# Kernel optimization log

Hardware: AMD Instinct MI355X
Metric: run time of the kernel (lower is better)

The kernel has to match this reference:

```python
import jax, jax.numpy as jnp
import numpy as np

ASSIGN_TEMP = 0.1
BATCH_SIZE = 16
NUM_PROTOTYPES = 1024
EMBD_DIM = 512


def setup_inputs() -> dict:
    key = jax.random.key(0)
    k1, k2 = jax.random.split(key)
    feature_maps = jax.random.normal(k1, (BATCH_SIZE, EMBD_DIM, 64, 64), dtype=jnp.float32)
    prototypes = jax.random.normal(k2, (1, NUM_PROTOTYPES, EMBD_DIM), dtype=jnp.float32)
    return {"feature_maps": feature_maps, "prototypes": prototypes}


def reference(feature_maps, prototypes):
    # assign_nearest_clusters
    bs, c, h, w = feature_maps.shape
    K = prototypes.shape[1]
    # [N, c] pixel embeddings (channels-last flatten, as movedim(1,3).reshape)
    x = feature_maps.transpose(0, 2, 3, 1).reshape(-1, c)
    p = prototypes[0]  # [K, c]
    d2 = (jnp.sum(x * x, axis=1, keepdims=True)
          + jnp.sum(p * p, axis=1)[None, :]
          - 2.0 * (x @ p.T))
    dist = jnp.sqrt(jnp.maximum(d2, 0.0))  # [N, K]
    sims = jax.nn.softmax(-dist / ASSIGN_TEMP, axis=1)  # [N, K]
    sims = sims.reshape(bs, h, w, K).transpose(0, 3, 1, 2)  # [bs, K, h, w]
    nearest = jnp.argmax(sims, axis=1)  # [bs, h, w]
    onehot = jax.nn.one_hot(nearest, K, dtype=jnp.int32)  # [bs, h, w, K]
    counts = onehot.sum(axis=(1, 2))  # [bs, K] pixels per prototype
    mask = (counts > 3).sum()
    return sims, mask.astype(jnp.float32) / BATCH_SIZE
```

## Files before the change

### kernel.cpp

```cpp
#include <hip/hip_runtime.h>
#include <hip/hip_bf16.h>
#include <stdint.h>

typedef _Float16 f16x8 __attribute__((ext_vector_type(8)));
typedef _Float16 f16x2 __attribute__((ext_vector_type(2)));
typedef float    f32x4 __attribute__((ext_vector_type(4)));

#define NPROTO 1024
#define EMB    512
#define NB     16
#define HW     4096
#define NPIX   (NB * HW)
#define INV_TEMP 10.0f
#define TPX    64
#define NTHR   1024

__global__ void prep_protos(const float* __restrict__ proto,
                            _Float16* __restrict__ Ph,
                            float* __restrict__ pnorm) {
    int k = blockIdx.x;
    int t = threadIdx.x;
    const float* src = proto + (size_t)k * EMB + t * 8;
    float4 v0 = ((const float4*)src)[0];
    float4 v1 = ((const float4*)src)[1];
    float sq = v0.x*v0.x + v0.y*v0.y + v0.z*v0.z + v0.w*v0.w
             + v1.x*v1.x + v1.y*v1.y + v1.z*v1.z + v1.w*v1.w;
    f16x8 h;
    h[0] = (_Float16)v0.x; h[1] = (_Float16)v0.y; h[2] = (_Float16)v0.z; h[3] = (_Float16)v0.w;
    h[4] = (_Float16)v1.x; h[5] = (_Float16)v1.y; h[6] = (_Float16)v1.z; h[7] = (_Float16)v1.w;
    *(f16x8*)(Ph + (size_t)k * EMB + t * 8) = h;
#pragma unroll
    for (int m = 1; m < 64; m <<= 1) sq += __shfl_xor(sq, m);
    if (t == 0) pnorm[k] = sq;
}

__global__ void zero_counts(int* __restrict__ counts) {
    int i = blockIdx.x * blockDim.x + threadIdx.x;
    if (i < NB * NPROTO) counts[i] = 0;
}

__global__ __launch_bounds__(NTHR)
void assign_main(const float* __restrict__ fm, const _Float16* __restrict__ Ph,
                 const float* __restrict__ pnorm, int* __restrict__ counts,
                 float* __restrict__ out) {
    __shared__ __align__(16) unsigned char smem[143360];
    unsigned char* Abuf = smem;
    unsigned char* Bbuf = smem + 131072;
    float* pn           = (float*)(smem + 139264);
    float* redmax = (float*)(smem);
    float* redsum = (float*)(smem + 4096);
    float* argv_  = (float*)(smem + 8192);
    int*   argk_  = (int*)  (smem + 12288);
    float* xnsum  = (float*)(smem + 16384);
    float* xn     = (float*)(smem + 20480);

    const int t    = threadIdx.x;
    const int lane = t & 63, wid = t >> 6;
    const int lrow = lane >> 4;
    const int lcol = lane & 15;

    const int n0  = blockIdx.x * TPX;
    const int b   = n0 >> 12;
    const int hw0 = n0 & 4095;

    pn[t] = pnorm[t];

    f32x4 acc[4][4];
#pragma unroll
    for (int i = 0; i < 4; ++i)
#pragma unroll
        for (int j = 0; j < 4; ++j)
#pragma unroll
            for (int e = 0; e < 4; ++e) acc[i][j][e] = 0.0f;

    const int bpx = t & 63;
    const int bc  = (t >> 6) << 1;
    const float* fmB = fm + (size_t)b * EMB * HW + hw0 + bpx;
    float sq = 0.0f;
    float bv0, bv1;

    auto stageA = [&](int cur, int ks) {
        const int c0 = ks * 32;
#pragma unroll
        for (int p = 0; p < 4; ++p) {
            int k  = p * 256 + wid * 16 + (lane >> 2);
            int cg = (lane & 3) ^ (k & 3);
            const _Float16* src = Ph + (size_t)k * EMB + c0 + cg * 8;
            __builtin_amdgcn_global_load_lds(
                (const __attribute__((address_space(1))) void*)src,
                (__attribute__((address_space(3))) void*)(Abuf + cur * 65536 + p * 16384 + wid * 1024),
                16, 0, 0);
        }
    };
    auto loadB = [&](int ks) {
        const float* p0 = fmB + (size_t)(ks * 32 + bc) * HW;
        bv0 = p0[0];
        bv1 = p0[HW];
    };
    auto writeB = [&](int cur) {
        sq += bv0 * bv0 + bv1 * bv1;
        f16x2 h; h[0] = (_Float16)bv0; h[1] = (_Float16)bv1;
        int slot = (bc >> 3) ^ (bpx & 3);
        *(f16x2*)(Bbuf + cur * 4096 + bpx * 64 + (slot << 4) + (bc & 7) * 2) = h;
    };

    stageA(0, 0);
    loadB(0);
    writeB(0);
    __syncthreads();

    int cur = 0;
    for (int ks = 0; ks < 16; ++ks) {
        if (ks < 15) {
            stageA(cur ^ 1, ks + 1);
            loadB(ks + 1);
        }
        f16x8 bf[4];
#pragma unroll
        for (int nf = 0; nf < 4; ++nf) {
            int px   = nf * 16 + lcol;
            int slot = lrow ^ (px & 3);
            bf[nf] = *(const f16x8*)(Bbuf + cur * 4096 + px * 64 + (slot << 4));
        }
#pragma unroll
        for (int mf = 0; mf < 4; ++mf) {
            int r    = wid * 64 + mf * 16 + lcol;
            int slot = lrow ^ (r & 3);
            f16x8 af = *(const f16x8*)(Abuf + cur * 65536 + r * 64 + (slot << 4));
#pragma unroll
            for (int nf = 0; nf < 4; ++nf)
                acc[mf][nf] = __builtin_amdgcn_mfma_f32_16x16x32_f16(af, bf[nf], acc[mf][nf], 0, 0, 0);
        }
        if (ks < 15) writeB(cur ^ 1);
        __syncthreads();
        cur ^= 1;
    }

    xnsum[(t >> 6) * 64 + bpx] = sq;
    __syncthreads();
    if (t < 64) {
        float s = 0.0f;
#pragma unroll
        for (int g = 0; g < 16; ++g) s += xnsum[g * 64 + t];
        xn[t] = s;
    }
    __syncthreads();

    float xnv[4];
#pragma unroll
    for (int nf = 0; nf < 4; ++nf) xnv[nf] = xn[nf * 16 + lcol];

    float lmax[4] = {-1e30f, -1e30f, -1e30f, -1e30f};
    float lav[4]  = {-1e30f, -1e30f, -1e30f, -1e30f};
    int   lak[4]  = {0, 0, 0, 0};
#pragma unroll
    for (int mf = 0; mf < 4; ++mf) {
#pragma unroll
        for (int nf = 0; nf < 4; ++nf) {
#pragma unroll
            for (int j = 0; j < 4; ++j) {
                int kidx = wid * 64 + mf * 16 + lrow * 4 + j;
                float d2 = xnv[nf] + pn[kidx] - 2.0f * acc[mf][nf][j];
                float lg = -INV_TEMP * sqrtf(fmaxf(d2, 0.0f));
                acc[mf][nf][j] = lg;
                if (lg > lav[nf]) { lav[nf] = lg; lak[nf] = kidx; }
                lmax[nf] = fmaxf(lmax[nf], lg);
            }
        }
    }
#pragma unroll
    for (int nf = 0; nf < 4; ++nf) {
#pragma unroll
        for (int m = 16; m <= 32; m <<= 1) {
            float ov = __shfl_xor(lav[nf], m);
            int   ok = __shfl_xor(lak[nf], m);
            if (ov > lav[nf] || (ov == lav[nf] && ok < lak[nf])) { lav[nf] = ov; lak[nf] = ok; }
            lmax[nf] = fmaxf(lmax[nf], __shfl_xor(lmax[nf], m));
        }
    }
    if (lane < 16) {
#pragma unroll
        for (int nf = 0; nf < 4; ++nf) {
            int idx = wid * 64 + nf * 16 + lane;
            redmax[idx] = lmax[nf];
            argv_[idx]  = lav[nf];
            argk_[idx]  = lak[nf];
        }
    }
    __syncthreads();

    float gmax[4];
#pragma unroll
    for (int nf = 0; nf < 4; ++nf) {
        int px = nf * 16 + lcol;
        float gm = -1e30f, gav = -1e30f;
        int gak = 0;
#pragma unroll
        for (int w = 0; w < 16; ++w) {
            gm = fmaxf(gm, redmax[w * 64 + px]);
            float av = argv_[w * 64 + px];
            int   ak = argk_[w * 64 + px];
            if (av > gav || (av == gav && ak < gak)) { gav = av; gak = ak; }
        }
        gmax[nf] = gm;
        if (wid == 0 && lane < 16) atomicAdd(&counts[b * NPROTO + gak], 1);

        float s = 0.0f;
#pragma unroll
        for (int mf = 0; mf < 4; ++mf)
#pragma unroll
            for (int j = 0; j < 4; ++j) {
                float e = __expf(acc[mf][nf][j] - gm);
                acc[mf][nf][j] = e;
                s += e;
            }
        s += __shfl_xor(s, 16);
        s += __shfl_xor(s, 32);
        if (lane < 16) redsum[wid * 64 + nf * 16 + lane] = s;
    }
    __syncthreads();

    const size_t obase = (size_t)b * NPROTO * HW + hw0;
#pragma unroll
    for (int nf = 0; nf < 4; ++nf) {
        int px = nf * 16 + lcol;
        float s = 0.0f;
#pragma unroll
        for (int w = 0; w < 16; ++w) s += redsum[w * 64 + px];
        float inv = 1.0f / s;
#pragma unroll
        for (int mf = 0; mf < 4; ++mf)
#pragma unroll
            for (int j = 0; j < 4; ++j) {
                int kidx = wid * 64 + mf * 16 + lrow * 4 + j;
                out[obase + (size_t)kidx * HW + px] = acc[mf][nf][j] * inv;
            }
    }
}

__global__ void finalize(const int* __restrict__ counts, float* __restrict__ out) {
    int t = threadIdx.x;
    int local = 0;
    for (int i = t; i < NB * NPROTO; i += 256) local += (counts[i] > 3) ? 1 : 0;
#pragma unroll
    for (int m = 1; m < 64; m <<= 1) local += __shfl_xor(local, m);
    __shared__ int wsum[4];
    if ((t & 63) == 0) wsum[t >> 6] = local;
    __syncthreads();
    if (t == 0) out[(size_t)NPIX * NPROTO] = (float)(wsum[0] + wsum[1] + wsum[2] + wsum[3]) / 16.0f;
}

extern "C" void kernel_launch(void* const* d_in, const int* in_sizes, int n_in,
                              void* d_out, int out_size, void* d_ws, size_t ws_size,
                              hipStream_t stream) {
    const float* fm    = (const float*)d_in[0];
    const float* proto = (const float*)d_in[1];
    float* out = (float*)d_out;

    char* ws = (char*)d_ws;
    _Float16* Ph     = (_Float16*)ws;
    float*    pnorm  = (float*)(ws + (size_t)NPROTO * EMB * 2);
    int*      counts = (int*)(ws + (size_t)NPROTO * EMB * 2 + 4096);

    prep_protos<<<NPROTO, 64, 0, stream>>>(proto, Ph, pnorm);
    zero_counts<<<(NB * NPROTO + 255) / 256, 256, 0, stream>>>(counts);
    assign_main<<<NPIX / TPX, NTHR, 0, stream>>>(fm, Ph, pnorm, counts, out);
    finalize<<<1, 256, 0, stream>>>(counts, out);
}
```

Measured before the change: 299.5 us.

## Split assignment into transpose, stats, and recompute-emit passes with coalesced output

Adds a pre-pass that transposes feature maps into a channels-last fp16 buffer along with pixel norms. A stats kernel then runs the GEMM to get the per-pixel max, inverse softmax sum and argmax counts, and an emit kernel recomputes the GEMM in 256x256 tiles, staging results through LDS so the output writes are coalesced float4 stores. The aim is to remove the poorly coalesced strided output stores and the scalar fp32 B loads of the fused kernel. The cost is a second full GEMM and a 64MB intermediate buffer. The new path runs only when the workspace is large enough, and the old fused kernel is kept as a fallback.

```diff
diff --git a/kernel.cpp b/kernel.cpp
--- a/kernel.cpp
+++ b/kernel.cpp
@@ -12,8 +12,6 @@
 #define HW     4096
 #define NPIX   (NB * HW)
 #define INV_TEMP 10.0f
-#define TPX    64
-#define NTHR   1024
 
 __global__ void prep_protos(const float* __restrict__ proto,
                             _Float16* __restrict__ Ph,
@@ -39,10 +37,314 @@
     if (i < NB * NPROTO) counts[i] = 0;
 }
 
-__global__ __launch_bounds__(NTHR)
-void assign_main(const float* __restrict__ fm, const _Float16* __restrict__ Ph,
-                 const float* __restrict__ pnorm, int* __restrict__ counts,
-                 float* __restrict__ out) {
+__global__ __launch_bounds__(1024)
+void p0_transpose(const float* __restrict__ fm, _Float16* __restrict__ Xh,
+                  float* __restrict__ xn) {
+    __shared__ __align__(16) unsigned char tile[128 * 1024];
+    __shared__ float xnpart[32 * 128];
+
+    const int t   = threadIdx.x;
+    const int b   = blockIdx.x >> 5;
+    const int px0 = (blockIdx.x & 31) * 128;
+
+    float sq0 = 0.f, sq1 = 0.f, sq2 = 0.f, sq3 = 0.f;
+    const int p4 = t & 31;
+#pragma unroll
+    for (int j = 0; j < 16; ++j) {
+        int f4 = j * 1024 + t;
+        int c  = f4 >> 5;
+        float4 v = *(const float4*)(fm + ((size_t)b * EMB + c) * HW + px0 + p4 * 4);
+        sq0 += v.x * v.x; sq1 += v.y * v.y; sq2 += v.z * v.z; sq3 += v.w * v.w;
+#pragma unroll
+        for (int i = 0; i < 4; ++i) {
+            int p = p4 * 4 + i;
+            float val = (i == 0) ? v.x : (i == 1) ? v.y : (i == 2) ? v.z : v.w;
+            int slot = (c >> 3) ^ ((p >> 2) & 63);
+            *(_Float16*)(tile + p * 1024 + slot * 16 + (c & 7) * 2) = (_Float16)val;
+        }
+    }
+    xnpart[(t >> 5) * 128 + p4 * 4 + 0] = sq0;
+    xnpart[(t >> 5) * 128 + p4 * 4 + 1] = sq1;
+    xnpart[(t >> 5) * 128 + p4 * 4 + 2] = sq2;
+    xnpart[(t >> 5) * 128 + p4 * 4 + 3] = sq3;
+    __syncthreads();
+
+    if (t < 128) {
+        float s = 0.f;
+#pragma unroll
+        for (int g = 0; g < 32; ++g) s += xnpart[g * 128 + t];
+        xn[b * HW + px0 + t] = s;
+    }
+    const int wid = t >> 6, lane = t & 63;
+#pragma unroll
+    for (int rr = 0; rr < 8; ++rr) {
+        int p = wid * 8 + rr;
+        int phys = lane ^ ((p >> 2) & 63);
+        f16x8 v = *(const f16x8*)(tile + p * 1024 + phys * 16);
+        *(f16x8*)(Xh + ((size_t)b * HW + px0 + p) * EMB + lane * 8) = v;
+    }
+}
+
+__global__ __launch_bounds__(1024, 4)
+void p1_stats(const _Float16* __restrict__ Xh, const _Float16* __restrict__ Ph,
+              const float* __restrict__ pnorm, const float* __restrict__ xn,
+              int* __restrict__ counts, float* __restrict__ m_g, float* __restrict__ rs_g) {
+    __shared__ __align__(16) unsigned char smem[143360];
+    unsigned char* Abuf = smem;
+    unsigned char* Bbuf = smem + 131072;
+    float* pn           = (float*)(smem + 139264);
+    float* redmax = (float*)(smem);
+    float* redsum = (float*)(smem + 4096);
+    float* argv_  = (float*)(smem + 8192);
+    int*   argk_  = (int*)  (smem + 12288);
+
+    const int t    = threadIdx.x;
+    const int lane = t & 63, wid = t >> 6;
+    const int lrow = lane >> 4, lcol = lane & 15;
+    const int n0   = blockIdx.x * 64;
+    const int b    = n0 >> 12;
+
+    pn[t] = pnorm[t];
+
+    f32x4 acc[4][4];
+#pragma unroll
+    for (int i = 0; i < 4; ++i)
+#pragma unroll
+        for (int j = 0; j < 4; ++j)
+#pragma unroll
+            for (int e = 0; e < 4; ++e) acc[i][j][e] = 0.0f;
+
+    auto stageA = [&](int cur, int ks) {
+        const int c0 = ks * 32;
+#pragma unroll
+        for (int p = 0; p < 4; ++p) {
+            int k  = p * 256 + wid * 16 + (lane >> 2);
+            int cg = (lane & 3) ^ (k & 3);
+            __builtin_amdgcn_global_load_lds(
+                (const __attribute__((address_space(1))) void*)(Ph + (size_t)k * EMB + c0 + cg * 8),
+                (__attribute__((address_space(3))) void*)(Abuf + cur * 65536 + p * 16384 + wid * 1024),
+                16, 0, 0);
+        }
+    };
+    auto stageB = [&](int cur, int ks) {
+        if (wid < 4) {
+            const int c0 = ks * 32;
+            int row = wid * 16 + (lane >> 2);
+            int cg  = (lane & 3) ^ (row & 3);
+            __builtin_amdgcn_global_load_lds(
+                (const __attribute__((address_space(1))) void*)(Xh + (size_t)(n0 + row) * EMB + c0 + cg * 8),
+                (__attribute__((address_space(3))) void*)(Bbuf + cur * 4096 + wid * 1024),
+                16, 0, 0);
+        }
+    };
+
+    stageA(0, 0); stageB(0, 0);
+    __syncthreads();
+
+    int cur = 0;
+    for (int ks = 0; ks < 16; ++ks) {
+        if (ks < 15) { stageA(cur ^ 1, ks + 1); stageB(cur ^ 1, ks + 1); }
+        f16x8 bf[4];
+#pragma unroll
+        for (int nf = 0; nf < 4; ++nf) {
+            int p = nf * 16 + lcol;
+            bf[nf] = *(const f16x8*)(Bbuf + cur * 4096 + p * 64 + ((lrow ^ (p & 3)) << 4));
+        }
+#pragma unroll
+        for (int mf = 0; mf < 4; ++mf) {
+            int r = wid * 64 + mf * 16 + lcol;
+            f16x8 af = *(const f16x8*)(Abuf + cur * 65536 + r * 64 + ((lrow ^ (r & 3)) << 4));
+#pragma unroll
+            for (int nf = 0; nf < 4; ++nf)
+                acc[mf][nf] = __builtin_amdgcn_mfma_f32_16x16x32_f16(af, bf[nf], acc[mf][nf], 0, 0, 0);
+        }
+        __syncthreads();
+        cur ^= 1;
+    }
+
+    float xnv[4];
+#pragma unroll
+    for (int nf = 0; nf < 4; ++nf) xnv[nf] = xn[n0 + nf * 16 + lcol];
+
+    float lmax[4] = {-1e30f, -1e30f, -1e30f, -1e30f};
+    float lav[4]  = {-1e30f, -1e30f, -1e30f, -1e30f};
+    int   lak[4]  = {0, 0, 0, 0};
+#pragma unroll
+    for (int mf = 0; mf < 4; ++mf)
+#pragma unroll
+        for (int nf = 0; nf < 4; ++nf)
+#pragma unroll
+            for (int j = 0; j < 4; ++j) {
+                int kidx = wid * 64 + mf * 16 + lrow * 4 + j;
+                float d2 = xnv[nf] + pn[kidx] - 2.0f * acc[mf][nf][j];
+                float lg = -INV_TEMP * sqrtf(fmaxf(d2, 0.0f));
+                acc[mf][nf][j] = lg;
+                if (lg > lav[nf]) { lav[nf] = lg; lak[nf] = kidx; }
+                lmax[nf] = fmaxf(lmax[nf], lg);
+            }
+#pragma unroll
+    for (int nf = 0; nf < 4; ++nf)
+#pragma unroll
+        for (int m = 16; m <= 32; m <<= 1) {
+            float ov = __shfl_xor(lav[nf], m);
+            int   ok = __shfl_xor(lak[nf], m);
+            if (ov > lav[nf] || (ov == lav[nf] && ok < lak[nf])) { lav[nf] = ov; lak[nf] = ok; }
+            lmax[nf] = fmaxf(lmax[nf], __shfl_xor(lmax[nf], m));
+        }
+    if (lane < 16)
+#pragma unroll
+        for (int nf = 0; nf < 4; ++nf) {
+            int idx = wid * 64 + nf * 16 + lane;
+            redmax[idx] = lmax[nf]; argv_[idx] = lav[nf]; argk_[idx] = lak[nf];
+        }
+    __syncthreads();
+
+#pragma unroll
+    for (int nf = 0; nf < 4; ++nf) {
+        int px = nf * 16 + lcol;
+        float gm = -1e30f, gav = -1e30f;
+        int gak = 0;
+#pragma unroll
+        for (int w = 0; w < 16; ++w) {
+            gm = fmaxf(gm, redmax[w * 64 + px]);
+            float av = argv_[w * 64 + px];
+            int   ak = argk_[w * 64 + px];
+            if (av > gav || (av == gav && ak < gak)) { gav = av; gak = ak; }
+        }
+        if (wid == 0 && lane < 16) atomicAdd(&counts[b * NPROTO + gak], 1);
+        float s = 0.0f;
+#pragma unroll
+        for (int mf = 0; mf < 4; ++mf)
+#pragma unroll
+            for (int j = 0; j < 4; ++j) s += __expf(acc[mf][nf][j] - gm);
+        s += __shfl_xor(s, 16);
+        s += __shfl_xor(s, 32);
+        if (lane < 16) redsum[wid * 64 + nf * 16 + lane] = s;
+    }
+    __syncthreads();
+
+    if (t < 64) {
+        float gm = -1e30f, s = 0.0f;
+#pragma unroll
+        for (int w = 0; w < 16; ++w) { gm = fmaxf(gm, redmax[w * 64 + t]); s += redsum[w * 64 + t]; }
+        m_g[n0 + t]  = gm;
+        rs_g[n0 + t] = 1.0f / s;
+    }
+}
+
+__global__ __launch_bounds__(1024, 4)
+void p2_emit(const _Float16* __restrict__ Xh, const _Float16* __restrict__ Ph,
+             const float* __restrict__ pnorm, const float* __restrict__ xn,
+             const float* __restrict__ m_g, const float* __restrict__ rs_g,
+             float* __restrict__ out) {
+    __shared__ __align__(16) unsigned char smem[139264];
+    unsigned char* Abuf = smem;
+    unsigned char* Bbuf = smem + 32768;
+    float* EP  = (float*)(smem + 65536);
+    float* pnl = (float*)(smem + 131072);
+    float* xnl = (float*)(smem + 135168);
+    float* ml  = (float*)(smem + 136192);
+    float* rsl = (float*)(smem + 137216);
+
+    const int t    = threadIdx.x;
+    const int lane = t & 63, wid = t >> 6;
+    const int kw = wid >> 2, pw = wid & 3;
+    const int lrow = lane >> 4, lcol = lane & 15;
+
+    const int b   = blockIdx.x >> 4;
+    const int pxc = (blockIdx.x & 15) * 256;
+    const int n0  = b * HW + pxc;
+
+    pnl[t] = pnorm[t];
+    if (t < 256) { xnl[t] = xn[n0 + t]; ml[t] = m_g[n0 + t]; rsl[t] = rs_g[n0 + t]; }
+
+    auto stage = [&](int cur, int kq, int cs) {
+        const int c0 = cs * 32;
+        int rl   = wid * 16 + (lane >> 2);
+        int slot = lane & 3;
+        int cgA  = slot ^ (rl & 3);
+        __builtin_amdgcn_global_load_lds(
+            (const __attribute__((address_space(1))) void*)(Ph + (size_t)(kq * 256 + rl) * EMB + c0 + cgA * 8),
+            (__attribute__((address_space(3))) void*)(Abuf + cur * 16384 + wid * 1024), 16, 0, 0);
+        __builtin_amdgcn_global_load_lds(
+            (const __attribute__((address_space(1))) void*)(Xh + (size_t)(n0 + rl) * EMB + c0 + cgA * 8),
+            (__attribute__((address_space(3))) void*)(Bbuf + cur * 16384 + wid * 1024), 16, 0, 0);
+    };
+
+    for (int kq = 0; kq < 4; ++kq) {
+        f32x4 acc[4][4];
+#pragma unroll
+        for (int i = 0; i < 4; ++i)
+#pragma unroll
+            for (int j = 0; j < 4; ++j)
+#pragma unroll
+                for (int e = 0; e < 4; ++e) acc[i][j][e] = 0.0f;
+
+        stage(0, kq, 0);
+        __syncthreads();
+        int cur = 0;
+        for (int cs = 0; cs < 16; ++cs) {
+            if (cs < 15) stage(cur ^ 1, kq, cs + 1);
+            f16x8 bf[4];
+#pragma unroll
+            for (int nf = 0; nf < 4; ++nf) {
+                int p = pw * 64 + nf * 16 + lcol;
+                bf[nf] = *(const f16x8*)(Bbuf + cur * 16384 + p * 64 + ((lrow ^ (p & 3)) << 4));
+            }
+#pragma unroll
+            for (int mf = 0; mf < 4; ++mf) {
+                int r = kw * 64 + mf * 16 + lcol;
+                f16x8 af = *(const f16x8*)(Abuf + cur * 16384 + r * 64 + ((lrow ^ (r & 3)) << 4));
+#pragma unroll
+                for (int nf = 0; nf < 4; ++nf)
+                    acc[mf][nf] = __builtin_amdgcn_mfma_f32_16x16x32_f16(af, bf[nf], acc[mf][nf], 0, 0, 0);
+            }
+            __syncthreads();
+            cur ^= 1;
+        }
+
+#pragma unroll
+        for (int mf = 0; mf < 4; ++mf) {
+#pragma unroll
+            for (int nf = 0; nf < 4; ++nf) {
+                int px_l = pw * 64 + nf * 16 + lcol;
+#pragma unroll
+                for (int j = 0; j < 4; ++j) {
+                    int k_g = kq * 256 + kw * 64 + mf * 16 + lrow * 4 + j;
+                    float d2 = xnl[px_l] + pnl[k_g] - 2.0f * acc[mf][nf][j];
+                    float lg = -INV_TEMP * sqrtf(fmaxf(d2, 0.0f));
+                    EP[kw * 4096 + (lrow * 4 + j) * 256 + px_l] = __expf(lg - ml[px_l]) * rsl[px_l];
+                }
+            }
+            __syncthreads();
+#pragma unroll
+            for (int rr = 0; rr < 4; ++rr) {
+                int row = pw * 4 + rr;
+                int k_g = kq * 256 + kw * 64 + mf * 16 + row;
+                f32x4 v = *(const f32x4*)(EP + kw * 4096 + row * 256 + lane * 4);
+                *(f32x4*)(out + ((size_t)(b * NPROTO + k_g)) * HW + pxc + lane * 4) = v;
+            }
+            __syncthreads();
+        }
+    }
+}
+
+__global__ void finalize(const int* __restrict__ counts, float* __restrict__ out) {
+    int t = threadIdx.x;
+    int local = 0;
+    for (int i = t; i < NB * NPROTO; i += 256) local += (counts[i] > 3) ? 1 : 0;
+#pragma unroll
+    for (int m = 1; m < 64; m <<= 1) local += __shfl_xor(local, m);
+    __shared__ int wsum[4];
+    if ((t & 63) == 0) wsum[t >> 6] = local;
+    __syncthreads();
+    if (t == 0) out[(size_t)NPIX * NPROTO] = (float)(wsum[0] + wsum[1] + wsum[2] + wsum[3]) / 16.0f;
+}
+
+__global__ __launch_bounds__(1024, 1)
+void assign_fused(const float* __restrict__ fm, const _Float16* __restrict__ Ph,
+                  const float* __restrict__ pnorm, int* __restrict__ counts,
+                  float* __restrict__ out) {
     __shared__ __align__(16) unsigned char smem[143360];
     unsigned char* Abuf = smem;
     unsigned char* Bbuf = smem + 131072;
@@ -56,15 +358,12 @@
 
     const int t    = threadIdx.x;
     const int lane = t & 63, wid = t >> 6;
-    const int lrow = lane >> 4;
-    const int lcol = lane & 15;
-
-    const int n0  = blockIdx.x * TPX;
+    const int lrow = lane >> 4, lcol = lane & 15;
+    const int n0  = blockIdx.x * 64;
     const int b   = n0 >> 12;
     const int hw0 = n0 & 4095;
 
     pn[t] = pnorm[t];
-
     f32x4 acc[4][4];
 #pragma unroll
     for (int i = 0; i < 4; ++i)
@@ -85,17 +384,15 @@
         for (int p = 0; p < 4; ++p) {
             int k  = p * 256 + wid * 16 + (lane >> 2);
             int cg = (lane & 3) ^ (k & 3);
-            const _Float16* src = Ph + (size_t)k * EMB + c0 + cg * 8;
             __builtin_amdgcn_global_load_lds(
-                (const __attribute__((address_space(1))) void*)src,
+                (const __attribute__((address_space(1))) void*)(Ph + (size_t)k * EMB + c0 + cg * 8),
                 (__attribute__((address_space(3))) void*)(Abuf + cur * 65536 + p * 16384 + wid * 1024),
                 16, 0, 0);
         }
     };
     auto loadB = [&](int ks) {
         const float* p0 = fmB + (size_t)(ks * 32 + bc) * HW;
-        bv0 = p0[0];
-        bv1 = p0[HW];
+        bv0 = p0[0]; bv1 = p0[HW];
     };
     auto writeB = [&](int cur) {
         sq += bv0 * bv0 + bv1 * bv1;
@@ -104,29 +401,21 @@
         *(f16x2*)(Bbuf + cur * 4096 + bpx * 64 + (slot << 4) + (bc & 7) * 2) = h;
     };
 
-    stageA(0, 0);
-    loadB(0);
-    writeB(0);
-    __syncthreads();
-
+    stageA(0, 0); loadB(0); writeB(0);
+    __syncthreads();
     int cur = 0;
     for (int ks = 0; ks < 16; ++ks) {
-        if (ks < 15) {
-            stageA(cur ^ 1, ks + 1);
-            loadB(ks + 1);
-        }
+        if (ks < 15) { stageA(cur ^ 1, ks + 1); loadB(ks + 1); }
         f16x8 bf[4];
 #pragma unroll
         for (int nf = 0; nf < 4; ++nf) {
-            int px   = nf * 16 + lcol;
-            int slot = lrow ^ (px & 3);
-            bf[nf] = *(const f16x8*)(Bbuf + cur * 4096 + px * 64 + (slot << 4));
+            int px = nf * 16 + lcol;
+            bf[nf] = *(const f16x8*)(Bbuf + cur * 4096 + px * 64 + ((lrow ^ (px & 3)) << 4));
         }
 #pragma unroll
         for (int mf = 0; mf < 4; ++mf) {
-            int r    = wid * 64 + mf * 16 + lcol;
-            int slot = lrow ^ (r & 3);
-            f16x8 af = *(const f16x8*)(Abuf + cur * 65536 + r * 64 + (slot << 4));
+            int r = wid * 64 + mf * 16 + lcol;
+            f16x8 af = *(const f16x8*)(Abuf + cur * 65536 + r * 64 + ((lrow ^ (r & 3)) << 4));
 #pragma unroll
             for (int nf = 0; nf < 4; ++nf)
                 acc[mf][nf] = __builtin_amdgcn_mfma_f32_16x16x32_f16(af, bf[nf], acc[mf][nf], 0, 0, 0);
@@ -149,14 +438,13 @@
     float xnv[4];
 #pragma unroll
     for (int nf = 0; nf < 4; ++nf) xnv[nf] = xn[nf * 16 + lcol];
-
     float lmax[4] = {-1e30f, -1e30f, -1e30f, -1e30f};
     float lav[4]  = {-1e30f, -1e30f, -1e30f, -1e30f};
     int   lak[4]  = {0, 0, 0, 0};
 #pragma unroll
-    for (int mf = 0; mf < 4; ++mf) {
-#pragma unroll
-        for (int nf = 0; nf < 4; ++nf) {
+    for (int mf = 0; mf < 4; ++mf)
+#pragma unroll
+        for (int nf = 0; nf < 4; ++nf)
 #pragma unroll
             for (int j = 0; j < 4; ++j) {
                 int kidx = wid * 64 + mf * 16 + lrow * 4 + j;
@@ -166,10 +454,8 @@
                 if (lg > lav[nf]) { lav[nf] = lg; lak[nf] = kidx; }
                 lmax[nf] = fmaxf(lmax[nf], lg);
             }
-        }
-    }
-#pragma unroll
-    for (int nf = 0; nf < 4; ++nf) {
+#pragma unroll
+    for (int nf = 0; nf < 4; ++nf)
 #pragma unroll
         for (int m = 16; m <= 32; m <<= 1) {
             float ov = __shfl_xor(lav[nf], m);
@@ -177,16 +463,12 @@
             if (ov > lav[nf] || (ov == lav[nf] && ok < lak[nf])) { lav[nf] = ov; lak[nf] = ok; }
             lmax[nf] = fmaxf(lmax[nf], __shfl_xor(lmax[nf], m));
         }
-    }
-    if (lane < 16) {
+    if (lane < 16)
 #pragma unroll
         for (int nf = 0; nf < 4; ++nf) {
             int idx = wid * 64 + nf * 16 + lane;
-            redmax[idx] = lmax[nf];
-            argv_[idx]  = lav[nf];
-            argk_[idx]  = lak[nf];
-        }
-    }
+            redmax[idx] = lmax[nf]; argv_[idx] = lav[nf]; argk_[idx] = lak[nf];
+        }
     __syncthreads();
 
     float gmax[4];
@@ -204,7 +486,6 @@
         }
         gmax[nf] = gm;
         if (wid == 0 && lane < 16) atomicAdd(&counts[b * NPROTO + gak], 1);
-
         float s = 0.0f;
 #pragma unroll
         for (int mf = 0; mf < 4; ++mf)
@@ -236,18 +517,6 @@
                 out[obase + (size_t)kidx * HW + px] = acc[mf][nf][j] * inv;
             }
     }
-}
-
-__global__ void finalize(const int* __restrict__ counts, float* __restrict__ out) {
-    int t = threadIdx.x;
-    int local = 0;
-    for (int i = t; i < NB * NPROTO; i += 256) local += (counts[i] > 3) ? 1 : 0;
-#pragma unroll
-    for (int m = 1; m < 64; m <<= 1) local += __shfl_xor(local, m);
-    __shared__ int wsum[4];
-    if ((t & 63) == 0) wsum[t >> 6] = local;
-    __syncthreads();
-    if (t == 0) out[(size_t)NPIX * NPROTO] = (float)(wsum[0] + wsum[1] + wsum[2] + wsum[3]) / 16.0f;
 }
 
 extern "C" void kernel_launch(void* const* d_in, const int* in_sizes, int n_in,
@@ -258,12 +527,37 @@
     float* out = (float*)d_out;
 
     char* ws = (char*)d_ws;
-    _Float16* Ph     = (_Float16*)ws;
-    float*    pnorm  = (float*)(ws + (size_t)NPROTO * EMB * 2);
-    int*      counts = (int*)(ws + (size_t)NPROTO * EMB * 2 + 4096);
-
-    prep_protos<<<NPROTO, 64, 0, stream>>>(proto, Ph, pnorm);
-    zero_counts<<<(NB * NPROTO + 255) / 256, 256, 0, stream>>>(counts);
-    assign_main<<<NPIX / TPX, NTHR, 0, stream>>>(fm, Ph, pnorm, counts, out);
-    finalize<<<1, 256, 0, stream>>>(counts, out);
-}
+    const size_t XH_OFF = 0;
+    const size_t XN_OFF = 67108864;
+    const size_t M_OFF  = 67371008;
+    const size_t RS_OFF = 67633152;
+    const size_t PN_OFF = 67895296;
+    const size_t CT_OFF = 67899392;
+    const size_t PH_OFF = 67964928;
+    const size_t NEED   = PH_OFF + 1048576;
+
+    if (ws_size >= NEED) {
+        _Float16* Xh    = (_Float16*)(ws + XH_OFF);
+        float*    xn    = (float*)(ws + XN_OFF);
+        float*    m_g   = (float*)(ws + M_OFF);
+        float*    rs_g  = (float*)(ws + RS_OFF);
+        float*    pnorm = (float*)(ws + PN_OFF);
+        int*      counts= (int*)(ws + CT_OFF);
+        _Float16* Ph    = (_Float16*)(ws + PH_OFF);
+
+        prep_protos<<<NPROTO, 64, 0, stream>>>(proto, Ph, pnorm);
+        zero_counts<<<(NB * NPROTO + 255) / 256, 256, 0, stream>>>(counts);
+        p0_transpose<<<NB * 32, 1024, 0, stream>>>(fm, Xh, xn);
+        p1_stats<<<NPIX / 64, 1024, 0, stream>>>(Xh, Ph, pnorm, xn, counts, m_g, rs_g);
+        p2_emit<<<NB * 16, 1024, 0, stream>>>(Xh, Ph, pnorm, xn, m_g, rs_g, out);
+        finalize<<<1, 256, 0, stream>>>(counts, out);
+    } else {
+        _Float16* Ph    = (_Float16*)ws;
+        float*    pnorm = (float*)(ws + (size_t)NPROTO * EMB * 2);
+        int*      counts= (int*)(ws + (size_t)NPROTO * EMB * 2 + 4096);
+        prep_protos<<<NPROTO, 64, 0, stream>>>(proto, Ph, pnorm);
+        zero_counts<<<(NB * NPROTO + 255) / 256, 256, 0, stream>>>(counts);
+        assign_fused<<<NPIX / 64, 1024, 0, stream>>>(fm, Ph, pnorm, counts, out);
+        finalize<<<1, 256, 0, stream>>>(counts, out);
+    }
+}
```

New measurement: 392.5 us. 1.31x slower.

## Split assignment into K-sliced GEMM, softmax-combine, and transposed emit kernels

Applied to the files above, without the earlier changes.

The single fused kernel gives way to a three-phase pipeline. A smaller GEMM kernel (512 threads, 4 prototype slices per 128-pixel tile, less shared memory) writes unnormalized fp16 exponentials plus per-slice max, sum and argmax stats. A combine kernel merges the slice stats into per-slice scale factors and histogram counts. An emit kernel rescales the values and transposes them through shared memory into coalesced fp32 output. The aim is higher occupancy and better overlap than the 1024-thread, 140KB-smem fused kernel, at the cost of a 128MB fp16 intermediate round trip and extra launches. The old fused path remains as a fallback when the workspace is too small.

```diff
diff --git a/kernel.cpp b/kernel.cpp
--- a/kernel.cpp
+++ b/kernel.cpp
@@ -3,6 +3,7 @@
 #include <stdint.h>
 
 typedef _Float16 f16x8 __attribute__((ext_vector_type(8)));
+typedef _Float16 f16x4 __attribute__((ext_vector_type(4)));
 typedef _Float16 f16x2 __attribute__((ext_vector_type(2)));
 typedef float    f32x4 __attribute__((ext_vector_type(4)));
 
@@ -12,8 +13,6 @@
 #define HW     4096
 #define NPIX   (NB * HW)
 #define INV_TEMP 10.0f
-#define TPX    64
-#define NTHR   1024
 
 __global__ void prep_protos(const float* __restrict__ proto,
                             _Float16* __restrict__ Ph,
@@ -39,10 +38,279 @@
     if (i < NB * NPROTO) counts[i] = 0;
 }
 
-__global__ __launch_bounds__(NTHR)
-void assign_main(const float* __restrict__ fm, const _Float16* __restrict__ Ph,
-                 const float* __restrict__ pnorm, int* __restrict__ counts,
-                 float* __restrict__ out) {
+__global__ __launch_bounds__(512, 4)
+void pA_gemm(const float* __restrict__ fm, const _Float16* __restrict__ Ph,
+             const float* __restrict__ pnorm,
+             _Float16* __restrict__ e_out, float4* __restrict__ pstat) {
+    __shared__ __align__(16) unsigned char Abuf[2 * 16384];
+    __shared__ __align__(16) unsigned char Bbuf[2 * 8192];
+    __shared__ float pn[256];
+    __shared__ float xnp[4 * 128];
+    __shared__ float xnl[128];
+    __shared__ float redmax[4 * 128];
+    __shared__ float redsum[4 * 128];
+    __shared__ float argv_[4 * 128];
+    __shared__ int   argk_[4 * 128];
+
+    const int t    = threadIdx.x;
+    const int lane = t & 63, wid = t >> 6;
+    const int kw   = wid >> 1, pw = wid & 1;
+    const int lrow = lane >> 4, lcol = lane & 15;
+
+    const int bid   = blockIdx.x;
+    const int pt    = bid >> 2, slice = bid & 3;
+    const int gpx0  = pt * 128;
+    const int b     = gpx0 >> 12;
+    const int hw0   = gpx0 & 4095;
+    const int k0g   = slice * 256;
+
+    if (t < 256) pn[t] = pnorm[k0g + t];
+
+    f32x4 acc[4][4];
+#pragma unroll
+    for (int i = 0; i < 4; ++i)
+#pragma unroll
+        for (int j = 0; j < 4; ++j)
+#pragma unroll
+            for (int e = 0; e < 4; ++e) acc[i][j][e] = 0.0f;
+
+    const int bpx = t & 127, bcg = t >> 7;
+    const float* fmB = fm + (size_t)b * EMB * HW + hw0 + bpx;
+    float bv[8];
+    float sq = 0.0f;
+
+    auto stageA = [&](int cur, int ks) {
+        const int c0 = ks * 32;
+#pragma unroll
+        for (int h = 0; h < 2; ++h) {
+            int r = wid * 32 + h * 16 + (lane >> 2);
+            const _Float16* src = Ph + (size_t)(k0g + r) * EMB + c0 + (lane & 3) * 8;
+            __builtin_amdgcn_global_load_lds(
+                (const __attribute__((address_space(1))) void*)src,
+                (__attribute__((address_space(3))) void*)(Abuf + cur * 16384 + wid * 2048 + h * 1024),
+                16, 0, 0);
+        }
+    };
+    auto loadB = [&](int ks) {
+        const int c0 = ks * 32 + bcg * 8;
+#pragma unroll
+        for (int i = 0; i < 8; ++i) bv[i] = fmB[(size_t)(c0 + i) * HW];
+    };
+    auto writeB = [&](int cur) {
+        f16x8 h;
+#pragma unroll
+        for (int i = 0; i < 8; ++i) { sq += bv[i] * bv[i]; h[i] = (_Float16)bv[i]; }
+        *(f16x8*)(Bbuf + cur * 8192 + bcg * 2048 + bpx * 16) = h;
+    };
+
+    stageA(0, 0); loadB(0); writeB(0);
+    __syncthreads();
+
+    int cur = 0;
+    for (int ks = 0; ks < 16; ++ks) {
+        if (ks < 15) { stageA(cur ^ 1, ks + 1); loadB(ks + 1); }
+        f16x8 bf[4];
+#pragma unroll
+        for (int nf = 0; nf < 4; ++nf) {
+            int px = pw * 64 + nf * 16 + lcol;
+            bf[nf] = *(const f16x8*)(Bbuf + cur * 8192 + lrow * 2048 + px * 16);
+        }
+#pragma unroll
+        for (int mf = 0; mf < 4; ++mf) {
+            int r = kw * 64 + mf * 16 + lcol;
+            f16x8 af = *(const f16x8*)(Abuf + cur * 16384 + r * 64 + lrow * 16);
+#pragma unroll
+            for (int nf = 0; nf < 4; ++nf)
+                acc[mf][nf] = __builtin_amdgcn_mfma_f32_16x16x32_f16(af, bf[nf], acc[mf][nf], 0, 0, 0);
+        }
+        if (ks < 15) writeB(cur ^ 1);
+        __syncthreads();
+        cur ^= 1;
+    }
+
+    xnp[bcg * 128 + bpx] = sq;
+    __syncthreads();
+    if (t < 128) {
+        float s = 0.0f;
+#pragma unroll
+        for (int g = 0; g < 4; ++g) s += xnp[g * 128 + t];
+        xnl[t] = s;
+    }
+    __syncthreads();
+
+    float xnv[4];
+#pragma unroll
+    for (int nf = 0; nf < 4; ++nf) xnv[nf] = xnl[pw * 64 + nf * 16 + lcol];
+
+    float lmax[4] = {-1e30f, -1e30f, -1e30f, -1e30f};
+    float lav[4]  = {-1e30f, -1e30f, -1e30f, -1e30f};
+    int   lak[4]  = {0, 0, 0, 0};
+#pragma unroll
+    for (int mf = 0; mf < 4; ++mf)
+#pragma unroll
+        for (int nf = 0; nf < 4; ++nf)
+#pragma unroll
+            for (int j = 0; j < 4; ++j) {
+                int kl = kw * 64 + mf * 16 + lrow * 4 + j;
+                float d2 = xnv[nf] + pn[kl] - 2.0f * acc[mf][nf][j];
+                float lg = -INV_TEMP * sqrtf(fmaxf(d2, 0.0f));
+                acc[mf][nf][j] = lg;
+                if (lg > lav[nf]) { lav[nf] = lg; lak[nf] = kl; }
+                lmax[nf] = fmaxf(lmax[nf], lg);
+            }
+#pragma unroll
+    for (int nf = 0; nf < 4; ++nf)
+#pragma unroll
+        for (int m = 16; m <= 32; m <<= 1) {
+            float ov = __shfl_xor(lav[nf], m);
+            int   ok = __shfl_xor(lak[nf], m);
+            if (ov > lav[nf] || (ov == lav[nf] && ok < lak[nf])) { lav[nf] = ov; lak[nf] = ok; }
+            lmax[nf] = fmaxf(lmax[nf], __shfl_xor(lmax[nf], m));
+        }
+    if (lane < 16)
+#pragma unroll
+        for (int nf = 0; nf < 4; ++nf) {
+            int px = pw * 64 + nf * 16 + lane;
+            redmax[kw * 128 + px] = lmax[nf];
+            argv_[kw * 128 + px]  = lav[nf];
+            argk_[kw * 128 + px]  = lak[nf];
+        }
+    __syncthreads();
+
+    float gm[4];
+#pragma unroll
+    for (int nf = 0; nf < 4; ++nf) {
+        int px = pw * 64 + nf * 16 + lcol;
+        float m = -1e30f;
+#pragma unroll
+        for (int w = 0; w < 4; ++w) m = fmaxf(m, redmax[w * 128 + px]);
+        gm[nf] = m;
+        float s = 0.0f;
+#pragma unroll
+        for (int mf = 0; mf < 4; ++mf)
+#pragma unroll
+            for (int j = 0; j < 4; ++j) {
+                float e = __expf(acc[mf][nf][j] - m);
+                acc[mf][nf][j] = e;
+                s += e;
+            }
+        s += __shfl_xor(s, 16);
+        s += __shfl_xor(s, 32);
+        if (lane < 16) redsum[kw * 128 + nf * 16 + pw * 64 + lane] = s;
+    }
+
+#pragma unroll
+    for (int mf = 0; mf < 4; ++mf)
+#pragma unroll
+        for (int nf = 0; nf < 4; ++nf) {
+            int px = pw * 64 + nf * 16 + lcol;
+            int kl = kw * 64 + mf * 16 + lrow * 4;
+            f16x4 h;
+#pragma unroll
+            for (int j = 0; j < 4; ++j) h[j] = (_Float16)acc[mf][nf][j];
+            *(f16x4*)(e_out + (size_t)(gpx0 + px) * NPROTO + k0g + kl) = h;
+        }
+    __syncthreads();
+
+    if (kw == 0 && lane < 16) {
+#pragma unroll
+        for (int nf = 0; nf < 4; ++nf) {
+            int px = pw * 64 + nf * 16 + lane;
+            float m = -1e30f, s = 0.0f, av = -1e30f;
+            int ak = 0;
+#pragma unroll
+            for (int w = 0; w < 4; ++w) {
+                m = fmaxf(m, redmax[w * 128 + px]);
+                s += redsum[w * 128 + px];
+                float v = argv_[w * 128 + px];
+                int   k = argk_[w * 128 + px];
+                if (v > av || (v == av && k < ak)) { av = v; ak = k; }
+            }
+            float4 st;
+            st.x = m; st.y = s; st.z = __int_as_float(k0g + ak); st.w = 0.0f;
+            pstat[(size_t)slice * NPIX + gpx0 + px] = st;
+        }
+    }
+}
+
+__global__ void pC_combine(const float4* __restrict__ pstat, float* __restrict__ scale,
+                           int* __restrict__ counts) {
+    int px = blockIdx.x * 256 + threadIdx.x;
+    if (px >= NPIX) return;
+    float4 s0 = pstat[px];
+    float4 s1 = pstat[NPIX + px];
+    float4 s2 = pstat[2 * NPIX + px];
+    float4 s3 = pstat[3 * NPIX + px];
+    float m = fmaxf(fmaxf(s0.x, s1.x), fmaxf(s2.x, s3.x));
+    float e0 = __expf(s0.x - m), e1 = __expf(s1.x - m);
+    float e2 = __expf(s2.x - m), e3 = __expf(s3.x - m);
+    float S = s0.y * e0 + s1.y * e1 + s2.y * e2 + s3.y * e3;
+    float rs = 1.0f / S;
+    scale[px * 4 + 0] = e0 * rs;
+    scale[px * 4 + 1] = e1 * rs;
+    scale[px * 4 + 2] = e2 * rs;
+    scale[px * 4 + 3] = e3 * rs;
+    float bv = s0.x; int bk = __float_as_int(s0.z);
+    if (s1.x > bv) { bv = s1.x; bk = __float_as_int(s1.z); }
+    if (s2.x > bv) { bv = s2.x; bk = __float_as_int(s2.z); }
+    if (s3.x > bv) { bv = s3.x; bk = __float_as_int(s3.z); }
+    int b = px >> 12;
+    atomicAdd(&counts[b * NPROTO + bk], 1);
+}
+
+__global__ __launch_bounds__(1024)
+void pB_emit(const _Float16* __restrict__ e, const float* __restrict__ scale,
+             float* __restrict__ out) {
+    __shared__ float tile[64 * 261];
+
+    const int t = threadIdx.x;
+    const int px0g = blockIdx.x * 256;
+    const int b = px0g >> 12, hw0 = px0g & 4095;
+    const int lpx = t >> 2, kq = t & 3;
+    const int orow = t >> 4, oseg = t & 15;
+
+    for (int kc = 0; kc < 16; ++kc) {
+        int slice = kc >> 2;
+        float sc = scale[(px0g + lpx) * 4 + slice];
+        const _Float16* src = e + (size_t)(px0g + lpx) * NPROTO + kc * 64 + kq * 16;
+        f16x8 h0 = *(const f16x8*)(src);
+        f16x8 h1 = *(const f16x8*)(src + 8);
+        if (kc) __syncthreads();
+#pragma unroll
+        for (int j = 0; j < 8; ++j) {
+            tile[(kq * 16 + j) * 261 + lpx]     = (float)h0[j] * sc;
+            tile[(kq * 16 + 8 + j) * 261 + lpx] = (float)h1[j] * sc;
+        }
+        __syncthreads();
+        size_t obase = (size_t)b * NPROTO * HW + (size_t)(kc * 64 + orow) * HW + hw0 + oseg * 16;
+#pragma unroll
+        for (int i = 0; i < 4; ++i) {
+            float4 v;
+            v.x = tile[orow * 261 + oseg * 16 + i * 4 + 0];
+            v.y = tile[orow * 261 + oseg * 16 + i * 4 + 1];
+            v.z = tile[orow * 261 + oseg * 16 + i * 4 + 2];
+            v.w = tile[orow * 261 + oseg * 16 + i * 4 + 3];
+            *(float4*)(out + obase + i * 4) = v;
+        }
+    }
+}
+
+__global__ void finalize(const int* __restrict__ counts, float* __restrict__ out) {
+    int t = threadIdx.x;
+    int local = 0;
+    for (int i = t; i < NB * NPROTO; i += 256) local += (counts[i] > 3) ? 1 : 0;
+#pragma unroll
+    for (int m = 1; m < 64; m <<= 1) local += __shfl_xor(local, m);
+    __shared__ int wsum[4];
+    if ((t & 63) == 0) wsum[t >> 6] = local;
+    __syncthreads();
+    if (t == 0) out[(size_t)NPIX * NPROTO] = (float)(wsum[0] + wsum[1] + wsum[2] + wsum[3]) / 16.0f;
+}
+
+__global__ __launch_bounds__(1024, 1)
+void assign_fused(const float* __restrict__ fm, const _Float16* __restrict__ Ph,
+                  const float* __restrict__ pnorm, int* __restrict__ counts,
+                  float* __restrict__ out) {
     __shared__ __align__(16) unsigned char smem[143360];
     unsigned char* Abuf = smem;
     unsigned char* Bbuf = smem + 131072;
@@ -56,15 +324,12 @@
 
     const int t    = threadIdx.x;
     const int lane = t & 63, wid = t >> 6;
-    const int lrow = lane >> 4;
-    const int lcol = lane & 15;
-
-    const int n0  = blockIdx.x * TPX;
+    const int lrow = lane >> 4, lcol = lane & 15;
+    const int n0  = blockIdx.x * 64;
     const int b   = n0 >> 12;
     const int hw0 = n0 & 4095;
 
     pn[t] = pnorm[t];
-
     f32x4 acc[4][4];
 #pragma unroll
     for (int i = 0; i < 4; ++i)
@@ -85,17 +350,15 @@
         for (int p = 0; p < 4; ++p) {
             int k  = p * 256 + wid * 16 + (lane >> 2);
             int cg = (lane & 3) ^ (k & 3);
-            const _Float16* src = Ph + (size_t)k * EMB + c0 + cg * 8;
             __builtin_amdgcn_global_load_lds(
-                (const __attribute__((address_space(1))) void*)src,
+                (const __attribute__((address_space(1))) void*)(Ph + (size_t)k * EMB + c0 + cg * 8),
                 (__attribute__((address_space(3))) void*)(Abuf + cur * 65536 + p * 16384 + wid * 1024),
                 16, 0, 0);
         }
     };
     auto loadB = [&](int ks) {
         const float* p0 = fmB + (size_t)(ks * 32 + bc) * HW;
-        bv0 = p0[0];
-        bv1 = p0[HW];
+        bv0 = p0[0]; bv1 = p0[HW];
     };
     auto writeB = [&](int cur) {
         sq += bv0 * bv0 + bv1 * bv1;
@@ -104,29 +367,21 @@
         *(f16x2*)(Bbuf + cur * 4096 + bpx * 64 + (slot << 4) + (bc & 7) * 2) = h;
     };
 
-    stageA(0, 0);
-    loadB(0);
-    writeB(0);
-    __syncthreads();
-
+    stageA(0, 0); loadB(0); writeB(0);
+    __syncthreads();
     int cur = 0;
     for (int ks = 0; ks < 16; ++ks) {
-        if (ks < 15) {
-            stageA(cur ^ 1, ks + 1);
-            loadB(ks + 1);
-        }
+        if (ks < 15) { stageA(cur ^ 1, ks + 1); loadB(ks + 1); }
         f16x8 bf[4];
 #pragma unroll
         for (int nf = 0; nf < 4; ++nf) {
-            int px   = nf * 16 + lcol;
-            int slot = lrow ^ (px & 3);
-            bf[nf] = *(const f16x8*)(Bbuf + cur * 4096 + px * 64 + (slot << 4));
+            int px = nf * 16 + lcol;
+            bf[nf] = *(const f16x8*)(Bbuf + cur * 4096 + px * 64 + ((lrow ^ (px & 3)) << 4));
         }
 #pragma unroll
         for (int mf = 0; mf < 4; ++mf) {
-            int r    = wid * 64 + mf * 16 + lcol;
-            int slot = lrow ^ (r & 3);
-            f16x8 af = *(const f16x8*)(Abuf + cur * 65536 + r * 64 + (slot << 4));
+            int r = wid * 64 + mf * 16 + lcol;
+            f16x8 af = *(const f16x8*)(Abuf + cur * 65536 + r * 64 + ((lrow ^ (r & 3)) << 4));
 #pragma unroll
             for (int nf = 0; nf < 4; ++nf)
                 acc[mf][nf] = __builtin_amdgcn_mfma_f32_16x16x32_f16(af, bf[nf], acc[mf][nf], 0, 0, 0);
@@ -149,14 +404,13 @@
     float xnv[4];
 #pragma unroll
     for (int nf = 0; nf < 4; ++nf) xnv[nf] = xn[nf * 16 + lcol];
-
     float lmax[4] = {-1e30f, -1e30f, -1e30f, -1e30f};
     float lav[4]  = {-1e30f, -1e30f, -1e30f, -1e30f};
     int   lak[4]  = {0, 0, 0, 0};
 #pragma unroll
-    for (int mf = 0; mf < 4; ++mf) {
-#pragma unroll
-        for (int nf = 0; nf < 4; ++nf) {
+    for (int mf = 0; mf < 4; ++mf)
+#pragma unroll
+        for (int nf = 0; nf < 4; ++nf)
 #pragma unroll
             for (int j = 0; j < 4; ++j) {
                 int kidx = wid * 64 + mf * 16 + lrow * 4 + j;
@@ -166,10 +420,8 @@
                 if (lg > lav[nf]) { lav[nf] = lg; lak[nf] = kidx; }
                 lmax[nf] = fmaxf(lmax[nf], lg);
             }
-        }
-    }
-#pragma unroll
-    for (int nf = 0; nf < 4; ++nf) {
+#pragma unroll
+    for (int nf = 0; nf < 4; ++nf)
 #pragma unroll
         for (int m = 16; m <= 32; m <<= 1) {
             float ov = __shfl_xor(lav[nf], m);
@@ -177,19 +429,14 @@
             if (ov > lav[nf] || (ov == lav[nf] && ok < lak[nf])) { lav[nf] = ov; lak[nf] = ok; }
             lmax[nf] = fmaxf(lmax[nf], __shfl_xor(lmax[nf], m));
         }
-    }
-    if (lane < 16) {
+    if (lane < 16)
 #pragma unroll
         for (int nf = 0; nf < 4; ++nf) {
             int idx = wid * 64 + nf * 16 + lane;
-            redmax[idx] = lmax[nf];
-            argv_[idx]  = lav[nf];
-            argk_[idx]  = lak[nf];
-        }
-    }
-    __syncthreads();
-
-    float gmax[4];
+            redmax[idx] = lmax[nf]; argv_[idx] = lav[nf]; argk_[idx] = lak[nf];
+        }
+    __syncthreads();
+
 #pragma unroll
     for (int nf = 0; nf < 4; ++nf) {
         int px = nf * 16 + lcol;
@@ -202,9 +449,7 @@
             int   ak = argk_[w * 64 + px];
             if (av > gav || (av == gav && ak < gak)) { gav = av; gak = ak; }
         }
-        gmax[nf] = gm;
         if (wid == 0 && lane < 16) atomicAdd(&counts[b * NPROTO + gak], 1);
-
         float s = 0.0f;
 #pragma unroll
         for (int mf = 0; mf < 4; ++mf)
@@ -238,18 +483,6 @@
     }
 }
 
-__global__ void finalize(const int* __restrict__ counts, float* __restrict__ out) {
-    int t = threadIdx.x;
-    int local = 0;
-    for (int i = t; i < NB * NPROTO; i += 256) local += (counts[i] > 3) ? 1 : 0;
-#pragma unroll
-    for (int m = 1; m < 64; m <<= 1) local += __shfl_xor(local, m);
-    __shared__ int wsum[4];
-    if ((t & 63) == 0) wsum[t >> 6] = local;
-    __syncthreads();
-    if (t == 0) out[(size_t)NPIX * NPROTO] = (float)(wsum[0] + wsum[1] + wsum[2] + wsum[3]) / 16.0f;
-}
-
 extern "C" void kernel_launch(void* const* d_in, const int* in_sizes, int n_in,
                               void* d_out, int out_size, void* d_ws, size_t ws_size,
                               hipStream_t stream) {
@@ -258,12 +491,35 @@
     float* out = (float*)d_out;
 
     char* ws = (char*)d_ws;
-    _Float16* Ph     = (_Float16*)ws;
-    float*    pnorm  = (float*)(ws + (size_t)NPROTO * EMB * 2);
-    int*      counts = (int*)(ws + (size_t)NPROTO * EMB * 2 + 4096);
-
-    prep_protos<<<NPROTO, 64, 0, stream>>>(proto, Ph, pnorm);
-    zero_counts<<<(NB * NPROTO + 255) / 256, 256, 0, stream>>>(counts);
-    assign_main<<<NPIX / TPX, NTHR, 0, stream>>>(fm, Ph, pnorm, counts, out);
-    finalize<<<1, 256, 0, stream>>>(counts, out);
-}
+    const size_t E_OFF  = 0;
+    const size_t PS_OFF = 134217728;
+    const size_t SC_OFF = PS_OFF + 4194304;
+    const size_t PH_OFF = SC_OFF + 1048576;
+    const size_t PN_OFF = PH_OFF + 1048576;
+    const size_t CT_OFF = PN_OFF + 4096;
+    const size_t NEED   = CT_OFF + 65536;
+
+    if (ws_size >= NEED) {
+        _Float16* e     = (_Float16*)(ws + E_OFF);
+        float4*   pstat = (float4*)(ws + PS_OFF);
+        float*    scale = (float*)(ws + SC_OFF);
+        _Float16* Ph    = (_Float16*)(ws + PH_OFF);
+        float*    pnorm = (float*)(ws + PN_OFF);
+        int*      counts= (int*)(ws + CT_OFF);
+
+        prep_protos<<<NPROTO, 64, 0, stream>>>(proto, Ph, pnorm);
+        zero_counts<<<(NB * NPROTO + 255) / 256, 256, 0, stream>>>(counts);
+        pA_gemm<<<(NPIX / 128) * 4, 512, 0, stream>>>(fm, Ph, pnorm, e, pstat);
+        pC_combine<<<NPIX / 256, 256, 0, stream>>>(pstat, scale, counts);
+        pB_emit<<<NPIX / 256, 1024, 0, stream>>>(e, scale, out);
+        finalize<<<1, 256, 0, stream>>>(counts, out);
+    } else {
+        _Float16* Ph    = (_Float16*)ws;
+        float*    pnorm = (float*)(ws + (size_t)NPROTO * EMB * 2);
+        int*      counts= (int*)(ws + (size_t)NPROTO * EMB * 2 + 4096);
+        prep_protos<<<NPROTO, 64, 0, stream>>>(proto, Ph, pnorm);
+        zero_counts<<<(NB * NPROTO + 255) / 256, 256, 0, stream>>>(counts);
+        assign_fused<<<NPIX / 64, 1024, 0, stream>>>(fm, Ph, pnorm, counts, out);
+        finalize<<<1, 256, 0, stream>>>(counts, out);
+    }
+}
```

After: 338.6 us (median of 2 runs). +13.1%, slower.
